# Optimization experiments

Hardware: AMD Instinct MI355X
Metric: run time of the kernel (lower is better)

## Reference

```python
import jax, jax.numpy as jnp
import numpy as np

B_, S_, D_, N_ = 4, 2048, 1024, 16

def setup_inputs() -> dict:
    key = jax.random.key(0)
    ks = jax.random.split(key, 8)
    x = jax.random.normal(ks[0], (B_, S_, D_), dtype=jnp.float32)
    A = jax.random.normal(ks[1], (D_, N_, N_), dtype=jnp.float32) * 0.1
    Bm = jax.random.normal(ks[2], (D_, N_), dtype=jnp.float32) * 0.1
    Cm = jax.random.normal(ks[3], (D_, N_), dtype=jnp.float32) * 0.1
    Dm = jax.random.normal(ks[4], (D_,), dtype=jnp.float32) * 0.1
    ln_w = jnp.ones((D_,), dtype=jnp.float32)
    ln_b = jnp.zeros((D_,), dtype=jnp.float32)
    W_out = jax.random.normal(ks[5], (D_, D_), dtype=jnp.float32) * (1.0 / np.sqrt(D_))
    b_out = jnp.zeros((D_,), dtype=jnp.float32)
    return {"x": x, "A": A, "Bm": Bm, "Cm": Cm, "Dm": Dm,
            "ln_w": ln_w, "ln_b": ln_b, "W_out": W_out, "b_out": b_out}

def _layernorm(y, w, b, eps=1e-5):
    mu = jnp.mean(y, axis=-1, keepdims=True)
    var = jnp.mean((y - mu) ** 2, axis=-1, keepdims=True)
    return (y - mu) * jax.lax.rsqrt(var + eps) * w + b

def reference(x, A, Bm, Cm, Dm, ln_w, ln_b, W_out, b_out):
    # x: [B, S, D]; per-channel SSM: h_t = A h_{t-1} + B x_t ; y_t = C.h_t + D x_t
    bsz = x.shape[0]
    h0 = jnp.zeros((bsz, A.shape[0], A.shape[1]), dtype=x.dtype)  # [B, D, N]

    def step(h, x_t):  # x_t: [B, D]
        h = jnp.einsum('dnm,bdm->bdn', A, h) + Bm[None] * x_t[..., None]
        y_t = jnp.einsum('dn,bdn->bd', Cm, h) + Dm * x_t
        return h, y_t

    _, y = jax.lax.scan(step, h0, jnp.swapaxes(x, 0, 1))  # y: [S, B, D]
    y = jnp.swapaxes(y, 0, 1)  # [B, S, D]
    y = _layernorm(y, ln_w, ln_b)
    y = jax.nn.gelu(y, approximate=False)
    y = y @ W_out.T + b_out
    return x + y
```

## Files before the change

### kernel.cpp

```cpp
#include <hip/hip_runtime.h>
#include <hip/hip_bf16.h>

#define D_DIM 1024
#define S_DIM 2048
#define B_DIM 4
#define KTAPS 16

typedef short bf16x8 __attribute__((ext_vector_type(8)));
typedef float f32x4 __attribute__((ext_vector_type(4)));
typedef short s16x8 __attribute__((ext_vector_type(8)));

#define GLOAD16(gptr, lptr) \
  __builtin_amdgcn_global_load_lds((const __attribute__((address_space(1))) unsigned int*)(gptr), \
                                   (__attribute__((address_space(3))) unsigned int*)(lptr), 16, 0, 0)

static __device__ __forceinline__ short f2bs(float f) {
  __hip_bfloat16 h = __float2bfloat16(f);
  return *reinterpret_cast<short*>(&h);
}

__global__ void taps_kernel(const float* __restrict__ A, const float* __restrict__ Bm,
                            const float* __restrict__ Cm, const float* __restrict__ Dm,
                            float* __restrict__ gT) {
  const int gb   = blockIdx.x;
  const int wid  = threadIdx.x >> 6;
  const int lane = threadIdx.x & 63;
  const int sub  = lane >> 4;
  const int n    = lane & 15;
  const int d    = gb * 16 + wid * 4 + sub;
  float Ar[16];
#pragma unroll
  for (int m = 0; m < 16; ++m) Ar[m] = A[d * 256 + n * 16 + m];
  float v = Bm[d * 16 + n];
  const float c   = Cm[d * 16 + n];
  const float dmv = Dm[d];
  const int base  = sub << 4;
  for (int k = 0; k < KTAPS; ++k) {
    float dot = c * v;
    dot += __shfl_xor(dot, 1);
    dot += __shfl_xor(dot, 2);
    dot += __shfl_xor(dot, 4);
    dot += __shfl_xor(dot, 8);
    if (k == 0) dot += dmv;
    if (n == 0) gT[k * D_DIM + d] = dot;
    float nv = 0.f;
#pragma unroll
    for (int m = 0; m < 16; ++m) nv = fmaf(Ar[m], __shfl(v, base + m), nv);
    v = nv;
  }
}

__global__ __launch_bounds__(256) void convln_kernel(const float* __restrict__ x,
                                                     const float* __restrict__ gT,
                                                     const float* __restrict__ lnw,
                                                     const float* __restrict__ lnb,
                                                     const float* __restrict__ W,
                                                     __hip_bfloat16* __restrict__ Wb,
                                                     __hip_bfloat16* __restrict__ act) {
  if (blockIdx.x >= 2048) {
    const int base = ((blockIdx.x - 2048) * 256 + threadIdx.x) * 8;
    const f32x4 w0 = *(const f32x4*)(W + base);
    const f32x4 w1 = *(const f32x4*)(W + base + 4);
    s16x8 o;
#pragma unroll
    for (int c = 0; c < 4; ++c) { o[c] = f2bs(w0[c]); o[4 + c] = f2bs(w1[c]); }
    *(s16x8*)((short*)Wb + base) = o;
    return;
  }

  __shared__ float redS[16];
  __shared__ float redQ[16];
  const int m0  = blockIdx.x * 4;
  const int b   = m0 >> 11;
  const int s0  = m0 & 2047;
  const int tid = threadIdx.x;
  const int lane = tid & 63, wid = tid >> 6;
  const int d0  = tid * 4;
  const float* xb = x + ((size_t)b * S_DIM) * D_DIM + d0;

  f32x4 w[19];
#pragma unroll
  for (int i = 0; i < 19; ++i) {
    const int s = s0 - 15 + i;
    w[i] = (s >= 0) ? *(const f32x4*)(xb + (size_t)s * D_DIM) : (f32x4){0.f, 0.f, 0.f, 0.f};
  }

  f32x4 a[4] = {(f32x4){0,0,0,0}, (f32x4){0,0,0,0}, (f32x4){0,0,0,0}, (f32x4){0,0,0,0}};
#pragma unroll
  for (int k = 0; k < KTAPS; ++k) {
    const f32x4 g4 = *(const f32x4*)(gT + k * D_DIM + d0);
#pragma unroll
    for (int j = 0; j < 4; ++j) {
      const f32x4 xv = w[15 + j - k];
#pragma unroll
      for (int c = 0; c < 4; ++c) a[j][c] = fmaf(g4[c], xv[c], a[j][c]);
    }
  }

#pragma unroll
  for (int j = 0; j < 4; ++j) {
    float s = a[j][0] + a[j][1] + a[j][2] + a[j][3];
    float q = a[j][0]*a[j][0] + a[j][1]*a[j][1] + a[j][2]*a[j][2] + a[j][3]*a[j][3];
    s += __shfl_xor(s, 1);  s += __shfl_xor(s, 2);  s += __shfl_xor(s, 4);
    s += __shfl_xor(s, 8);  s += __shfl_xor(s, 16); s += __shfl_xor(s, 32);
    q += __shfl_xor(q, 1);  q += __shfl_xor(q, 2);  q += __shfl_xor(q, 4);
    q += __shfl_xor(q, 8);  q += __shfl_xor(q, 16); q += __shfl_xor(q, 32);
    if (lane == 0) { redS[j * 4 + wid] = s; redQ[j * 4 + wid] = q; }
  }
  __syncthreads();

  const f32x4 w4 = *(const f32x4*)&lnw[d0];
  const f32x4 b4 = *(const f32x4*)&lnb[d0];
#pragma unroll
  for (int j = 0; j < 4; ++j) {
    const float sum = redS[j*4+0] + redS[j*4+1] + redS[j*4+2] + redS[j*4+3];
    const float sq  = redQ[j*4+0] + redQ[j*4+1] + redQ[j*4+2] + redQ[j*4+3];
    const float mu  = sum * (1.0f / D_DIM);
    const float var = sq * (1.0f / D_DIM) - mu * mu;
    const float inv = rsqrtf(var + 1e-5f);
    short4 o;
    short* op = &o.x;
#pragma unroll
    for (int c = 0; c < 4; ++c) {
      float t = (a[j][c] - mu) * inv * w4[c] + b4[c];
      float ge = 0.5f * t * (1.f + erff(t * 0.70710678118654752f));
      op[c] = f2bs(ge);
    }
    *(short4*)((short*)act + (size_t)(m0 + j) * D_DIM + d0) = o;
  }
}

__global__ __launch_bounds__(256, 2) void gemm_kernel(const __hip_bfloat16* __restrict__ Act,
                                                      const __hip_bfloat16* __restrict__ Wb,
                                                      const float* __restrict__ x,
                                                      const float* __restrict__ bout,
                                                      float* __restrict__ out) {
  __shared__ short Al[128 * 128];
  __shared__ short Bl[128 * 128];
  const int tid  = threadIdx.x;
  const int lane = tid & 63;
  const int wave = tid >> 6;
  const int mBase = blockIdx.x * 128;
  const int nBase = blockIdx.y * 128;
  const int wm = (wave & 1) * 64;
  const int wn = (wave >> 1) * 64;
  const int l16 = lane & 15;
  const int kq  = lane >> 4;
  const int r0  = kq * 4;

  const int srow = tid >> 4;
  const int cg   = (tid & 15) ^ (srow & 7);
  const short* Ag = (const short*)Act + (mBase + srow) * D_DIM + cg * 8;
  const short* Bg = (const short*)Wb  + (nBase + srow) * D_DIM + cg * 8;
  short* Als = Al + tid * 8;
  short* Bls = Bl + tid * 8;

  f32x4 acc[4][4];
#pragma unroll
  for (int mt = 0; mt < 4; ++mt)
#pragma unroll
    for (int nt = 0; nt < 4; ++nt) acc[mt][nt] = (f32x4){0.f, 0.f, 0.f, 0.f};

  f32x4 xr[4][4];
  float bo4[4];

  for (int k0 = 0; k0 < D_DIM; k0 += 128) {
    __syncthreads();
#pragma unroll
    for (int r = 0; r < 8; ++r) {
      GLOAD16(Ag + r * 16 * D_DIM + k0, Als + r * 2048);
      GLOAD16(Bg + r * 16 * D_DIM + k0, Bls + r * 2048);
    }
    __syncthreads();

    if (k0 == D_DIM - 128) {
#pragma unroll
      for (int nt = 0; nt < 4; ++nt) {
        const int col = nBase + wn + nt * 16 + l16;
        bo4[nt] = bout[col];
#pragma unroll
        for (int mt = 0; mt < 4; ++mt) {
          const int row = mBase + wm + mt * 16 + r0;
#pragma unroll
          for (int r = 0; r < 4; ++r)
            xr[mt][nt][r] = x[(size_t)(row + r) * D_DIM + col];
        }
      }
    }

#pragma unroll
    for (int kk = 0; kk < 128; kk += 32) {
      bf16x8 af[4], bfr[4];
      const int cgr = (kk >> 3) + kq;
#pragma unroll
      for (int mt = 0; mt < 4; ++mt) {
        const int r = wm + mt * 16 + l16;
        af[mt] = *(const bf16x8*)&Al[r * 128 + ((cgr ^ (r & 7)) << 3)];
      }
#pragma unroll
      for (int nt = 0; nt < 4; ++nt) {
        const int r = wn + nt * 16 + l16;
        bfr[nt] = *(const bf16x8*)&Bl[r * 128 + ((cgr ^ (r & 7)) << 3)];
      }
#pragma unroll
      for (int mt = 0; mt < 4; ++mt)
#pragma unroll
        for (int nt = 0; nt < 4; ++nt)
          acc[mt][nt] = __builtin_amdgcn_mfma_f32_16x16x32_bf16(af[mt], bfr[nt], acc[mt][nt], 0, 0, 0);
    }
  }

#pragma unroll
  for (int mt = 0; mt < 4; ++mt) {
    const int row = mBase + wm + mt * 16 + r0;
#pragma unroll
    for (int nt = 0; nt < 4; ++nt) {
      const int col = nBase + wn + nt * 16 + l16;
#pragma unroll
      for (int r = 0; r < 4; ++r) {
        const size_t idx = (size_t)(row + r) * D_DIM + col;
        __builtin_nontemporal_store(xr[mt][nt][r] + acc[mt][nt][r] + bo4[nt], &out[idx]);
      }
    }
  }
}

extern "C" void kernel_launch(void* const* d_in, const int* in_sizes, int n_in,
                              void* d_out, int out_size, void* d_ws, size_t ws_size,
                              hipStream_t stream) {
  const float* x    = (const float*)d_in[0];
  const float* A    = (const float*)d_in[1];
  const float* Bm   = (const float*)d_in[2];
  const float* Cm   = (const float*)d_in[3];
  const float* Dm   = (const float*)d_in[4];
  const float* lnw  = (const float*)d_in[5];
  const float* lnb  = (const float*)d_in[6];
  const float* Wout = (const float*)d_in[7];
  const float* bout = (const float*)d_in[8];
  float* out = (float*)d_out;

  char* ws = (char*)d_ws;
  float* gT            = (float*)ws;
  __hip_bfloat16* Wb   = (__hip_bfloat16*)(ws + 262144);
  __hip_bfloat16* Act  = (__hip_bfloat16*)(ws + 2359296);

  taps_kernel<<<64, 256, 0, stream>>>(A, Bm, Cm, Dm, gT);
  convln_kernel<<<2560, 256, 0, stream>>>(x, gT, lnw, lnb, Wout, Wb, Act);
  gemm_kernel<<<dim3(64, 8), 256, 0, stream>>>(Act, Wb, x, bout, out);
}
```

Before: 151.5 us.

## Shrink GEMM tiles to 128x64 with BK=64 for higher occupancy

The output GEMM tile goes from 128x128 with K-step 128 to 128x64 with K-step 64. This cuts LDS use and accumulator registers so four blocks can share a CU, and doubles the grid to 1024 blocks. The residual x prefetch in the last K iteration is removed, so x and the bias are loaded directly in the epilogue. In exchange, each block reuses less data, makes more K-loop iterations with barriers, and loads more A-tile data overall.

```diff
diff --git a/kernel.cpp b/kernel.cpp
--- a/kernel.cpp
+++ b/kernel.cpp
@@ -130,96 +130,80 @@
   }
 }
 
-__global__ __launch_bounds__(256, 2) void gemm_kernel(const __hip_bfloat16* __restrict__ Act,
+__global__ __launch_bounds__(256, 4) void gemm_kernel(const __hip_bfloat16* __restrict__ Act,
                                                       const __hip_bfloat16* __restrict__ Wb,
                                                       const float* __restrict__ x,
                                                       const float* __restrict__ bout,
                                                       float* __restrict__ out) {
-  __shared__ short Al[128 * 128];
-  __shared__ short Bl[128 * 128];
+  __shared__ short Al[128 * 64];
+  __shared__ short Bl[64 * 64];
   const int tid  = threadIdx.x;
   const int lane = tid & 63;
   const int wave = tid >> 6;
   const int mBase = blockIdx.x * 128;
-  const int nBase = blockIdx.y * 128;
+  const int nBase = blockIdx.y * 64;
   const int wm = (wave & 1) * 64;
-  const int wn = (wave >> 1) * 64;
+  const int wn = (wave >> 1) * 32;
   const int l16 = lane & 15;
   const int kq  = lane >> 4;
-  const int r0  = kq * 4;
-
-  const int srow = tid >> 4;
-  const int cg   = (tid & 15) ^ (srow & 7);
-  const short* Ag = (const short*)Act + (mBase + srow) * D_DIM + cg * 8;
-  const short* Bg = (const short*)Wb  + (nBase + srow) * D_DIM + cg * 8;
+
+  const int st = tid >> 3;
+  const int cg = (tid & 7) ^ (st & 7);
+  const short* Ag = (const short*)Act + (size_t)(mBase + st) * D_DIM + cg * 8;
+  const short* Bg = (const short*)Wb  + (size_t)(nBase + st) * D_DIM + cg * 8;
   short* Als = Al + tid * 8;
   short* Bls = Bl + tid * 8;
 
-  f32x4 acc[4][4];
+  f32x4 acc[4][2];
 #pragma unroll
   for (int mt = 0; mt < 4; ++mt)
 #pragma unroll
-    for (int nt = 0; nt < 4; ++nt) acc[mt][nt] = (f32x4){0.f, 0.f, 0.f, 0.f};
-
-  f32x4 xr[4][4];
-  float bo4[4];
-
-  for (int k0 = 0; k0 < D_DIM; k0 += 128) {
+    for (int nt = 0; nt < 2; ++nt) acc[mt][nt] = (f32x4){0.f, 0.f, 0.f, 0.f};
+
+  for (int k0 = 0; k0 < D_DIM; k0 += 64) {
     __syncthreads();
 #pragma unroll
-    for (int r = 0; r < 8; ++r) {
-      GLOAD16(Ag + r * 16 * D_DIM + k0, Als + r * 2048);
-      GLOAD16(Bg + r * 16 * D_DIM + k0, Bls + r * 2048);
-    }
+    for (int r = 0; r < 4; ++r)
+      GLOAD16(Ag + (size_t)r * 32 * D_DIM + k0, Als + r * 2048);
+#pragma unroll
+    for (int r = 0; r < 2; ++r)
+      GLOAD16(Bg + (size_t)r * 32 * D_DIM + k0, Bls + r * 2048);
     __syncthreads();
 
-    if (k0 == D_DIM - 128) {
-#pragma unroll
-      for (int nt = 0; nt < 4; ++nt) {
-        const int col = nBase + wn + nt * 16 + l16;
-        bo4[nt] = bout[col];
-#pragma unroll
-        for (int mt = 0; mt < 4; ++mt) {
-          const int row = mBase + wm + mt * 16 + r0;
-#pragma unroll
-          for (int r = 0; r < 4; ++r)
-            xr[mt][nt][r] = x[(size_t)(row + r) * D_DIM + col];
-        }
-      }
-    }
-
-#pragma unroll
-    for (int kk = 0; kk < 128; kk += 32) {
-      bf16x8 af[4], bfr[4];
+#pragma unroll
+    for (int kk = 0; kk < 64; kk += 32) {
+      bf16x8 af[4], bfr[2];
       const int cgr = (kk >> 3) + kq;
 #pragma unroll
       for (int mt = 0; mt < 4; ++mt) {
         const int r = wm + mt * 16 + l16;
-        af[mt] = *(const bf16x8*)&Al[r * 128 + ((cgr ^ (r & 7)) << 3)];
+        af[mt] = *(const bf16x8*)&Al[r * 64 + ((cgr ^ (r & 7)) << 3)];
       }
 #pragma unroll
-      for (int nt = 0; nt < 4; ++nt) {
+      for (int nt = 0; nt < 2; ++nt) {
         const int r = wn + nt * 16 + l16;
-        bfr[nt] = *(const bf16x8*)&Bl[r * 128 + ((cgr ^ (r & 7)) << 3)];
+        bfr[nt] = *(const bf16x8*)&Bl[r * 64 + ((cgr ^ (r & 7)) << 3)];
       }
 #pragma unroll
       for (int mt = 0; mt < 4; ++mt)
 #pragma unroll
-        for (int nt = 0; nt < 4; ++nt)
+        for (int nt = 0; nt < 2; ++nt)
           acc[mt][nt] = __builtin_amdgcn_mfma_f32_16x16x32_bf16(af[mt], bfr[nt], acc[mt][nt], 0, 0, 0);
     }
   }
 
+  const int r0 = kq * 4;
 #pragma unroll
   for (int mt = 0; mt < 4; ++mt) {
     const int row = mBase + wm + mt * 16 + r0;
 #pragma unroll
-    for (int nt = 0; nt < 4; ++nt) {
+    for (int nt = 0; nt < 2; ++nt) {
       const int col = nBase + wn + nt * 16 + l16;
+      const float bo = bout[col];
 #pragma unroll
       for (int r = 0; r < 4; ++r) {
         const size_t idx = (size_t)(row + r) * D_DIM + col;
-        __builtin_nontemporal_store(xr[mt][nt][r] + acc[mt][nt][r] + bo4[nt], &out[idx]);
+        __builtin_nontemporal_store(x[idx] + acc[mt][nt][r] + bo, &out[idx]);
       }
     }
   }
@@ -246,5 +230,5 @@
 
   taps_kernel<<<64, 256, 0, stream>>>(A, Bm, Cm, Dm, gT);
   convln_kernel<<<2560, 256, 0, stream>>>(x, gT, lnw, lnb, Wout, Wb, Act);
-  gemm_kernel<<<dim3(64, 8), 256, 0, stream>>>(Act, Wb, x, bout, out);
-}
+  gemm_kernel<<<dim3(64, 16), 256, 0, stream>>>(Act, Wb, x, bout, out);
+}
```

New measurement: 154.1 us. No clear change (+1.7%).
